# Performance work log

Hardware: AMD Instinct MI355X
Metric: run time of the kernel (lower is better)

Reference implementation:

```python
import jax, jax.numpy as jnp
import numpy as np

NUM_HEADS = 16
D_MODEL = 1024
D_K = D_MODEL // NUM_HEADS
EPS = 1e-6


def setup_inputs() -> dict:
    key = jax.random.key(0)
    ks = jax.random.split(key, 12)
    B, S, D = 8, 1024, D_MODEL
    scale = 0.02
    return {
        "query": jax.random.normal(ks[0], (B, S, D), dtype=jnp.float32),
        "key": jax.random.normal(ks[1], (B, S, D), dtype=jnp.float32),
        "value": jax.random.normal(ks[2], (B, S, D), dtype=jnp.float32),
        "policy": jax.random.uniform(ks[3], (B, S, 1), dtype=jnp.float32),
        "wq_w": jax.random.normal(ks[4], (D, D), dtype=jnp.float32) * scale,
        "wq_b": jnp.zeros((D,), dtype=jnp.float32),
        "wk_w": jax.random.normal(ks[5], (D, D), dtype=jnp.float32) * scale,
        "wk_b": jnp.zeros((D,), dtype=jnp.float32),
        "wv_w": jax.random.normal(ks[6], (D, D), dtype=jnp.float32) * scale,
        "wv_b": jnp.zeros((D,), dtype=jnp.float32),
        "dense_w": jax.random.normal(ks[7], (D, D), dtype=jnp.float32) * scale,
        "dense_b": jnp.zeros((D,), dtype=jnp.float32),
    }


def _split_heads(x):
    B, S, D = x.shape
    return x.reshape(B, S, NUM_HEADS, D_K).transpose(0, 2, 1, 3)  # [B,H,S,dk]


def reference(query, key, value, policy, wq_w, wq_b, wk_w, wk_b, wv_w, wv_b, dense_w, dense_b):
    B, S, D = query.shape
    # torch Linear: y = x @ W.T + b
    q = _split_heads(query @ wq_w.T + wq_b)
    k = _split_heads(key @ wk_w.T + wk_b)
    v = _split_heads(value @ wv_w.T + wv_b)

    scores = jnp.einsum("bhqd,bhkd->bhqk", q, k) / jnp.sqrt(jnp.float32(D_K))
    # policy branch: exp * policy normalization (no softmax max-subtraction, faithful)
    attn_policy = policy.reshape(B, 1, 1, S)
    sc = jnp.exp(scores) * attn_policy
    p_attn = (sc + EPS / S) / (jnp.sum(sc, axis=-1, keepdims=True) + EPS)

    x = jnp.einsum("bhqk,bhkd->bhqd", p_attn, v)
    x = x.transpose(0, 2, 1, 3).reshape(B, S, D)
    out = x @ dense_w.T + dense_b  # dropout = identity (eval mode)
    return out
```

## Files before the change

kernel.cpp:

```cpp
#include <hip/hip_runtime.h>


#define Sdim 1024
#define Ddim 1024

typedef unsigned short u16;
typedef float f32x4 __attribute__((ext_vector_type(4)));
typedef __bf16 bf16x8 __attribute__((ext_vector_type(8)));
typedef u16 u16x8 __attribute__((ext_vector_type(8)));
typedef __attribute__((address_space(3))) void lds_void;
typedef __attribute__((address_space(1))) void gbl_void;

__device__ __forceinline__ u16 f2bf(float f) {
    unsigned u = __float_as_uint(f);
    u += 0x7fffu + ((u >> 16) & 1u);
    return (u16)(u >> 16);
}
__device__ __forceinline__ void gld16(const void* g, void* l) {
    __builtin_amdgcn_global_load_lds((const gbl_void*)g, (lds_void*)l, 16, 0, 0);
}
#define MFMA16(a, b, c) __builtin_amdgcn_mfma_f32_16x16x32_bf16((a), (b), (c), 0, 0, 0)

__global__ __launch_bounds__(256) void cvt3(const float* __restrict__ s0,
                                            const float* __restrict__ s1,
                                            const float* __restrict__ s2,
                                            u16* __restrict__ d0,
                                            u16* __restrict__ d1,
                                            u16* __restrict__ d2) {
    const int z = blockIdx.y;
    const float* s = z == 0 ? s0 : z == 1 ? s1 : s2;
    u16* d = z == 0 ? d0 : z == 1 ? d1 : d2;
    const int i = (blockIdx.x * 256 + threadIdx.x) * 8;
    const float4 a = *(const float4*)(s + i);
    const float4 b = *(const float4*)(s + i + 4);
    u16x8 o;
    o[0] = f2bf(a.x); o[1] = f2bf(a.y); o[2] = f2bf(a.z); o[3] = f2bf(a.w);
    o[4] = f2bf(b.x); o[5] = f2bf(b.y); o[6] = f2bf(b.z); o[7] = f2bf(b.w);
    *(u16x8*)(d + i) = o;
}
__global__ __launch_bounds__(256) void cvt4(const float* __restrict__ s0,
                                            const float* __restrict__ s1,
                                            const float* __restrict__ s2,
                                            const float* __restrict__ s3,
                                            u16* __restrict__ d0,
                                            u16* __restrict__ d1,
                                            u16* __restrict__ d2,
                                            u16* __restrict__ d3) {
    const int z = blockIdx.y;
    const float* s = z == 0 ? s0 : z == 1 ? s1 : z == 2 ? s2 : s3;
    u16* d = z == 0 ? d0 : z == 1 ? d1 : z == 2 ? d2 : d3;
    const int i = (blockIdx.x * 256 + threadIdx.x) * 8;
    const float4 a = *(const float4*)(s + i);
    const float4 b = *(const float4*)(s + i + 4);
    u16x8 o;
    o[0] = f2bf(a.x); o[1] = f2bf(a.y); o[2] = f2bf(a.z); o[3] = f2bf(a.w);
    o[4] = f2bf(b.x); o[5] = f2bf(b.y); o[6] = f2bf(b.z); o[7] = f2bf(b.w);
    *(u16x8*)(d + i) = o;
}

template <bool OUT_BF16>
__device__ __forceinline__ void gemm_body(const u16* __restrict__ A,
                                          const u16* __restrict__ W,
                                          const float* __restrict__ bias,
                                          void* __restrict__ Cout,
                                          u16* As, u16* Bs,
                                          int m0, int n0) {
    const int tid  = threadIdx.x;
    const int wave = tid >> 6;
    const int lane = tid & 63;
    const int l15  = lane & 15;
    const int quad = lane >> 4;
    const int wm = (wave >> 1) * 64;
    const int wn = (wave & 1) * 64;

    const int e0 = wave * 512 + lane * 8;
    const int r0 = e0 >> 5, c0 = e0 & 31;
    const int e1 = 2048 + e0;
    const int r1 = e1 >> 5, c1 = e1 & 31;
    const u16* Ag0 = A + (size_t)(m0 + r0) * Ddim + c0;
    const u16* Ag1 = A + (size_t)(m0 + r1) * Ddim + c1;
    const u16* Wg0 = W + (size_t)(n0 + r0) * Ddim + c0;
    const u16* Wg1 = W + (size_t)(n0 + r1) * Ddim + c1;
    u16* As0 = As + wave * 512;
    u16* As1 = As + 2048 + wave * 512;
    u16* Bs0 = Bs + wave * 512;
    u16* Bs1 = Bs + 2048 + wave * 512;

    f32x4 acc[4][4] = {};

    for (int k0 = 0; k0 < Ddim; k0 += 32) {
        __syncthreads();
        gld16(Ag0 + k0, As0);
        gld16(Ag1 + k0, As1);
        gld16(Wg0 + k0, Bs0);
        gld16(Wg1 + k0, Bs1);
        __syncthreads();
        bf16x8 af[4], bfr[4];
#pragma unroll
        for (int i = 0; i < 4; ++i)
            af[i] = *(const bf16x8*)(As + (wm + i * 16 + l15) * 32 + quad * 8);
#pragma unroll
        for (int j = 0; j < 4; ++j)
            bfr[j] = *(const bf16x8*)(Bs + (wn + j * 16 + l15) * 32 + quad * 8);
#pragma unroll
        for (int i = 0; i < 4; ++i)
#pragma unroll
            for (int j = 0; j < 4; ++j)
                acc[i][j] = MFMA16(af[i], bfr[j], acc[i][j]);
    }

    float bv[4];
#pragma unroll
    for (int j = 0; j < 4; ++j) bv[j] = bias[n0 + wn + j * 16 + l15];
#pragma unroll
    for (int i = 0; i < 4; ++i)
#pragma unroll
        for (int j = 0; j < 4; ++j)
#pragma unroll
            for (int r = 0; r < 4; ++r) {
                const int row = m0 + wm + i * 16 + quad * 4 + r;
                const int col = n0 + wn + j * 16 + l15;
                const float v = acc[i][j][r] + bv[j];
                if (OUT_BF16)
                    ((u16*)Cout)[(size_t)row * Ddim + col] = f2bf(v);
                else
                    ((float*)Cout)[(size_t)row * Ddim + col] = v;
            }
}

__global__ __launch_bounds__(256) void gemm_qkv(const u16* __restrict__ A0, const u16* __restrict__ A1,
                                                const u16* __restrict__ A2,
                                                const u16* __restrict__ W0, const u16* __restrict__ W1,
                                                const u16* __restrict__ W2,
                                                const float* __restrict__ b0, const float* __restrict__ b1,
                                                const float* __restrict__ b2,
                                                u16* __restrict__ C0, u16* __restrict__ C1,
                                                u16* __restrict__ C2) {
    __shared__ __align__(16) u16 As[128 * 32];
    __shared__ __align__(16) u16 Bs[128 * 32];
    const int z = blockIdx.z;
    const u16* A = z == 0 ? A0 : z == 1 ? A1 : A2;
    const u16* W = z == 0 ? W0 : z == 1 ? W1 : W2;
    const float* bias = z == 0 ? b0 : z == 1 ? b1 : b2;
    u16* C = z == 0 ? C0 : z == 1 ? C1 : C2;
    gemm_body<true>(A, W, bias, (void*)C, As, Bs, blockIdx.x * 128, blockIdx.y * 128);
}

__global__ __launch_bounds__(256) void gemm_dense(const u16* __restrict__ A,
                                                  const u16* __restrict__ W,
                                                  const float* __restrict__ bias,
                                                  float* __restrict__ C) {
    __shared__ __align__(16) u16 As[128 * 32];
    __shared__ __align__(16) u16 Bs[128 * 32];
    gemm_body<false>(A, W, bias, (void*)C, As, Bs, blockIdx.x * 128, blockIdx.y * 128);
}

__global__ __launch_bounds__(256) void transp_v(const u16* __restrict__ Vp,
                                                u16* __restrict__ Vt) {
    __shared__ __align__(16) u16 Ts[64][72];
    const int bh = blockIdx.x, s0 = blockIdx.y * 64;
    const int b = bh >> 4, h = bh & 15;
    const int tid = threadIdx.x;
#pragma unroll
    for (int p = 0; p < 2; ++p) {
        const int e = p * 2048 + tid * 8;
        const int r = e >> 6, c = e & 63;
        *(u16x8*)&Ts[r][c] =
            *(const u16x8*)(Vp + ((size_t)(b * Sdim + s0 + r)) * Ddim + h * 64 + c);
    }
    __syncthreads();
    const int d = tid >> 2, sp = tid & 3;
#pragma unroll
    for (int g = 0; g < 2; ++g) {
        u16x8 o;
#pragma unroll
        for (int j = 0; j < 8; ++j) o[j] = Ts[sp * 16 + g * 8 + j][d];
        *(u16x8*)(Vt + ((size_t)(bh * 64 + d)) * Sdim + s0 + sp * 16 + g * 8) = o;
    }
}

__global__ __launch_bounds__(256) void attn_mfma(const u16* __restrict__ Qp,
                                                 const u16* __restrict__ Kp,
                                                 const u16* __restrict__ Vt,
                                                 const float* __restrict__ pol,
                                                 u16* __restrict__ Xb) {
    __shared__ __align__(16) u16 lds[29184];
    u16* Qs = lds;
    u16* Ks = lds + 4096;
    u16* Vs = lds + 12288;
    u16* Pg = lds + 20480;
    float* Xred = (float*)(lds + 4096);
    u16* XbR = lds + 20480;
    float* denb = (float*)(lds + 28672);
    float* pols = (float*)(lds + 28928);

    const int tid  = threadIdx.x;
    const int wave = tid >> 6;
    const int lane = tid & 63;
    const int l15  = lane & 15;
    const int quad = lane >> 4;
    const int wm = wave >> 1;
    const int wn = wave & 1;
    const int q0 = blockIdx.x * 64;
    const int bh = blockIdx.y;
    const int b = bh >> 4;
    const size_t bS = (size_t)b * Sdim;
    const int col0 = (bh & 15) * 64;
    const int lr4 = lane >> 2;
    const int lc8 = (lane & 3) * 8;

#pragma unroll
    for (int ks = 0; ks < 2; ++ks)
        gld16(Qp + (bS + q0 + wave * 16 + lr4) * Ddim + col0 + ks * 32 + lc8,
              Qs + (ks * 64 + wave * 16) * 32);

    f32x4 xacc[2][4] = {};
    float den[2][4] = {};

    for (int kt = 0; kt < 8; ++kt) {
        const int kbase = kt * 128;
        __syncthreads();
#pragma unroll
        for (int ks = 0; ks < 2; ++ks)
#pragma unroll
            for (int tt = 0; tt < 2; ++tt) {
                const int rblk = wave * 2 + tt;
                gld16(Kp + (bS + kbase + rblk * 16 + lr4) * Ddim + col0 + ks * 32 + lc8,
                      Ks + (ks * 128 + rblk * 16) * 32);
            }
#pragma unroll
        for (int tt = 0; tt < 4; ++tt)
            gld16(Vt + ((size_t)(bh * 64 + tt * 16 + lr4)) * Sdim + kbase + wave * 32 + lc8,
                  Vs + (wave * 64 + tt * 16) * 32);
        if (tid < 128) pols[tid] = pol[bS + kbase + tid];
        __syncthreads();

        bf16x8 aq[2][2];
#pragma unroll
        for (int i = 0; i < 2; ++i)
#pragma unroll
            for (int ks = 0; ks < 2; ++ks)
                aq[i][ks] = *(const bf16x8*)(Qs + (ks * 64 + wm * 32 + i * 16 + l15) * 32 + quad * 8);
#pragma unroll
        for (int i = 0; i < 2; ++i)
#pragma unroll
            for (int nt = 0; nt < 4; ++nt) {
                f32x4 sc = {};
#pragma unroll
                for (int ks = 0; ks < 2; ++ks) {
                    const bf16x8 bk =
                        *(const bf16x8*)(Ks + (ks * 128 + wn * 64 + nt * 16 + l15) * 32 + quad * 8);
                    sc = MFMA16(aq[i][ks], bk, sc);
                }
                const float pl = pols[wn * 64 + nt * 16 + l15];
#pragma unroll
                for (int r = 0; r < 4; ++r) {
                    const float p = __expf(sc[r] * 0.125f) * pl;
                    den[i][r] += p;
                    Pg[(((wave * 2 + i) * 2 + (nt >> 1)) * 16 + quad * 4 + r) * 32 +
                       (nt & 1) * 16 + l15] = f2bf(p);
                }
            }
#pragma unroll
        for (int i = 0; i < 2; ++i) {
            bf16x8 ap[2];
#pragma unroll
            for (int ks = 0; ks < 2; ++ks)
                ap[ks] = *(const bf16x8*)(Pg + (((wave * 2 + i) * 2 + ks) * 16 + l15) * 32 + quad * 8);
#pragma unroll
            for (int nd = 0; nd < 4; ++nd)
#pragma unroll
                for (int ks = 0; ks < 2; ++ks) {
                    const bf16x8 bv =
                        *(const bf16x8*)(Vs + ((wn * 2 + ks) * 64 + nd * 16 + l15) * 32 + quad * 8);
                    xacc[i][nd] = MFMA16(ap[ks], bv, xacc[i][nd]);
                }
        }
    }

    __syncthreads();

#pragma unroll
    for (int m = 1; m < 16; m <<= 1)
#pragma unroll
        for (int i = 0; i < 2; ++i)
#pragma unroll
            for (int r = 0; r < 4; ++r)
                den[i][r] += __shfl_xor(den[i][r], m, 64);
    if (l15 == 0)
#pragma unroll
        for (int i = 0; i < 2; ++i)
#pragma unroll
            for (int r = 0; r < 4; ++r)
                denb[wn * 64 + wm * 32 + i * 16 + quad * 4 + r] = den[i][r];
    if (wn == 1)
#pragma unroll
        for (int i = 0; i < 2; ++i)
#pragma unroll
            for (int nd = 0; nd < 4; ++nd)
#pragma unroll
                for (int r = 0; r < 4; ++r)
                    Xred[(wm * 32 + i * 16 + quad * 4 + r) * 68 + nd * 16 + l15] = xacc[i][nd][r];
    __syncthreads();

    if (wn == 0) {
#pragma unroll
        for (int i = 0; i < 2; ++i) {
            float inv[4];
#pragma unroll
            for (int r = 0; r < 4; ++r) {
                const int row = wm * 32 + i * 16 + quad * 4 + r;
                inv[r] = 1.0f / (denb[row] + denb[64 + row] + 1e-6f);
            }
#pragma unroll
            for (int nd = 0; nd < 4; ++nd)
#pragma unroll
                for (int r = 0; r < 4; ++r) {
                    const int row = wm * 32 + i * 16 + quad * 4 + r;
                    const float x = xacc[i][nd][r] + Xred[row * 68 + nd * 16 + l15];
                    XbR[row * 64 + nd * 16 + l15] = f2bf(x * inv[r]);
                }
        }
    }
    __syncthreads();

#pragma unroll
    for (int g = 0; g < 2; ++g) {
        const int e = g * 2048 + tid * 8;
        const int rr = e >> 6, cc = e & 63;
        const u16x8 o = *(const u16x8*)(XbR + rr * 64 + cc);
        *(u16x8*)(Xb + (bS + q0 + rr) * Ddim + col0 + cc) = o;
    }
}

extern "C" void kernel_launch(void* const* d_in, const int* in_sizes, int n_in,
                              void* d_out, int out_size, void* d_ws, size_t ws_size,
                              hipStream_t stream) {
    const float* query   = (const float*)d_in[0];
    const float* key     = (const float*)d_in[1];
    const float* value   = (const float*)d_in[2];
    const float* policy  = (const float*)d_in[3];
    const float* wq_w    = (const float*)d_in[4];
    const float* wq_b    = (const float*)d_in[5];
    const float* wk_w    = (const float*)d_in[6];
    const float* wk_b    = (const float*)d_in[7];
    const float* wv_w    = (const float*)d_in[8];
    const float* wv_b    = (const float*)d_in[9];
    const float* dense_w = (const float*)d_in[10];
    const float* dense_b = (const float*)d_in[11];

    const size_t MM = 1u << 20;
    const size_t A8 = 8 * MM;
    u16* qa  = (u16*)d_ws;
    u16* ka  = qa + A8;
    u16* va  = ka + A8;
    u16* wqb = va + A8;
    u16* wkb = wqb + MM;
    u16* wvb = wkb + MM;
    u16* wdb = wvb + MM;
    u16* Qp  = wdb + MM;
    u16* Kp  = Qp + A8;
    u16* Vp  = Kp + A8;
    u16* Vtg = ka;
    u16* Xb  = qa;

    cvt3<<<dim3(4096, 3), 256, 0, stream>>>(query, key, value, qa, ka, va);
    cvt4<<<dim3(512, 4), 256, 0, stream>>>(wq_w, wk_w, wv_w, dense_w, wqb, wkb, wvb, wdb);

    gemm_qkv<<<dim3(64, 8, 3), 256, 0, stream>>>(qa, ka, va, wqb, wkb, wvb,
                                                 wq_b, wk_b, wv_b, Qp, Kp, Vp);
    transp_v<<<dim3(128, 16), 256, 0, stream>>>(Vp, Vtg);

    attn_mfma<<<dim3(16, 128), 256, 0, stream>>>(Qp, Kp, Vtg, policy, Xb);

    gemm_dense<<<dim3(64, 8), 256, 0, stream>>>(Xb, wdb, dense_b, (float*)d_out);
}
```

Measured before the change: 353.8 us.

## Rework attention kernel with 32x32 MFMA, register-resident P and 256-row Q tiles

```diff
diff --git a/kernel.cpp b/kernel.cpp
--- a/kernel.cpp
+++ b/kernel.cpp
@@ -6,6 +6,7 @@
 
 typedef unsigned short u16;
 typedef float f32x4 __attribute__((ext_vector_type(4)));
+typedef float f32x16 __attribute__((ext_vector_type(16)));
 typedef __bf16 bf16x8 __attribute__((ext_vector_type(8)));
 typedef u16 u16x8 __attribute__((ext_vector_type(8)));
 typedef __attribute__((address_space(3))) void lds_void;
@@ -19,49 +20,45 @@
 __device__ __forceinline__ void gld16(const void* g, void* l) {
     __builtin_amdgcn_global_load_lds((const gbl_void*)g, (lds_void*)l, 16, 0, 0);
 }
+__device__ __forceinline__ unsigned pk_bf16(float lo, float hi) {
+    const unsigned ul = __float_as_uint(lo) + 0x8000u;
+    const unsigned uh = __float_as_uint(hi) + 0x8000u;
+    return __builtin_amdgcn_perm(uh, ul, 0x07060302u);
+}
 #define MFMA16(a, b, c) __builtin_amdgcn_mfma_f32_16x16x32_bf16((a), (b), (c), 0, 0, 0)
-
-__global__ __launch_bounds__(256) void cvt3(const float* __restrict__ s0,
-                                            const float* __restrict__ s1,
-                                            const float* __restrict__ s2,
-                                            u16* __restrict__ d0,
-                                            u16* __restrict__ d1,
-                                            u16* __restrict__ d2) {
+#define MFMA32(a, b, c) __builtin_amdgcn_mfma_f32_32x32x16_bf16((a), (b), (c), 0, 0, 0)
+
+__global__ __launch_bounds__(256) void cvt_all(const float* __restrict__ s0,
+                                               const float* __restrict__ s1,
+                                               const float* __restrict__ s2,
+                                               const float* __restrict__ s3,
+                                               const float* __restrict__ s4,
+                                               const float* __restrict__ s5,
+                                               const float* __restrict__ s6,
+                                               u16* __restrict__ d0, u16* __restrict__ d1,
+                                               u16* __restrict__ d2, u16* __restrict__ d3,
+                                               u16* __restrict__ d4, u16* __restrict__ d5,
+                                               u16* __restrict__ d6) {
     const int z = blockIdx.y;
-    const float* s = z == 0 ? s0 : z == 1 ? s1 : s2;
-    u16* d = z == 0 ? d0 : z == 1 ? d1 : d2;
+    if (z >= 3 && blockIdx.x >= 512) return;
+    const float* s = z == 0 ? s0 : z == 1 ? s1 : z == 2 ? s2 : z == 3 ? s3
+                   : z == 4 ? s4 : z == 5 ? s5 : s6;
+    u16* d = z == 0 ? d0 : z == 1 ? d1 : z == 2 ? d2 : z == 3 ? d3
+           : z == 4 ? d4 : z == 5 ? d5 : d6;
+    const float sc = (z == 3) ? 0.125f : 1.0f;
     const int i = (blockIdx.x * 256 + threadIdx.x) * 8;
     const float4 a = *(const float4*)(s + i);
     const float4 b = *(const float4*)(s + i + 4);
     u16x8 o;
-    o[0] = f2bf(a.x); o[1] = f2bf(a.y); o[2] = f2bf(a.z); o[3] = f2bf(a.w);
-    o[4] = f2bf(b.x); o[5] = f2bf(b.y); o[6] = f2bf(b.z); o[7] = f2bf(b.w);
-    *(u16x8*)(d + i) = o;
-}
-__global__ __launch_bounds__(256) void cvt4(const float* __restrict__ s0,
-                                            const float* __restrict__ s1,
-                                            const float* __restrict__ s2,
-                                            const float* __restrict__ s3,
-                                            u16* __restrict__ d0,
-                                            u16* __restrict__ d1,
-                                            u16* __restrict__ d2,
-                                            u16* __restrict__ d3) {
-    const int z = blockIdx.y;
-    const float* s = z == 0 ? s0 : z == 1 ? s1 : z == 2 ? s2 : s3;
-    u16* d = z == 0 ? d0 : z == 1 ? d1 : z == 2 ? d2 : d3;
-    const int i = (blockIdx.x * 256 + threadIdx.x) * 8;
-    const float4 a = *(const float4*)(s + i);
-    const float4 b = *(const float4*)(s + i + 4);
-    u16x8 o;
-    o[0] = f2bf(a.x); o[1] = f2bf(a.y); o[2] = f2bf(a.z); o[3] = f2bf(a.w);
-    o[4] = f2bf(b.x); o[5] = f2bf(b.y); o[6] = f2bf(b.z); o[7] = f2bf(b.w);
+    o[0] = f2bf(a.x * sc); o[1] = f2bf(a.y * sc); o[2] = f2bf(a.z * sc); o[3] = f2bf(a.w * sc);
+    o[4] = f2bf(b.x * sc); o[5] = f2bf(b.y * sc); o[6] = f2bf(b.z * sc); o[7] = f2bf(b.w * sc);
     *(u16x8*)(d + i) = o;
 }
 
 template <bool OUT_BF16>
 __device__ __forceinline__ void gemm_body(const u16* __restrict__ A,
                                           const u16* __restrict__ W,
-                                          const float* __restrict__ bias,
+                                          const float* __restrict__ bias, float bscale,
                                           void* __restrict__ Cout,
                                           u16* As, u16* Bs,
                                           int m0, int n0) {
@@ -111,7 +108,7 @@
 
     float bv[4];
 #pragma unroll
-    for (int j = 0; j < 4; ++j) bv[j] = bias[n0 + wn + j * 16 + l15];
+    for (int j = 0; j < 4; ++j) bv[j] = bias[n0 + wn + j * 16 + l15] * bscale;
 #pragma unroll
     for (int i = 0; i < 4; ++i)
 #pragma unroll
@@ -143,7 +140,8 @@
     const u16* W = z == 0 ? W0 : z == 1 ? W1 : W2;
     const float* bias = z == 0 ? b0 : z == 1 ? b1 : b2;
     u16* C = z == 0 ? C0 : z == 1 ? C1 : C2;
-    gemm_body<true>(A, W, bias, (void*)C, As, Bs, blockIdx.x * 128, blockIdx.y * 128);
+    const float bsc = (z == 0) ? 0.125f : 1.0f;
+    gemm_body<true>(A, W, bias, bsc, (void*)C, As, Bs, blockIdx.x * 128, blockIdx.y * 128);
 }
 
 __global__ __launch_bounds__(256) void gemm_dense(const u16* __restrict__ A,
@@ -152,7 +150,7 @@
                                                   float* __restrict__ C) {
     __shared__ __align__(16) u16 As[128 * 32];
     __shared__ __align__(16) u16 Bs[128 * 32];
-    gemm_body<false>(A, W, bias, (void*)C, As, Bs, blockIdx.x * 128, blockIdx.y * 128);
+    gemm_body<false>(A, W, bias, 1.0f, (void*)C, As, Bs, blockIdx.x * 128, blockIdx.y * 128);
 }
 
 __global__ __launch_bounds__(256) void transp_v(const u16* __restrict__ Vp,
@@ -179,157 +177,148 @@
     }
 }
 
-__global__ __launch_bounds__(256) void attn_mfma(const u16* __restrict__ Qp,
-                                                 const u16* __restrict__ Kp,
-                                                 const u16* __restrict__ Vt,
-                                                 const float* __restrict__ pol,
-                                                 u16* __restrict__ Xb) {
-    __shared__ __align__(16) u16 lds[29184];
+__global__ __launch_bounds__(256, 2) void attn_mfma(const u16* __restrict__ Qp,
+                                                    const u16* __restrict__ Kp,
+                                                    const u16* __restrict__ Vt,
+                                                    const float* __restrict__ pol,
+                                                    u16* __restrict__ Xb) {
+    __shared__ __align__(16) u16 lds[28288];
     u16* Qs = lds;
-    u16* Ks = lds + 4096;
-    u16* Vs = lds + 12288;
-    u16* Pg = lds + 20480;
-    float* Xred = (float*)(lds + 4096);
-    u16* XbR = lds + 20480;
-    float* denb = (float*)(lds + 28672);
-    float* pols = (float*)(lds + 28928);
+    u16* Ks = lds + 18432;
+    u16* Vs = lds + 23040;
+    float* pols = (float*)(lds + 27648);
+    float* denb = pols + 64;
 
     const int tid  = threadIdx.x;
-    const int wave = tid >> 6;
+    const int w    = tid >> 6;
     const int lane = tid & 63;
-    const int l15  = lane & 15;
-    const int quad = lane >> 4;
-    const int wm = wave >> 1;
-    const int wn = wave & 1;
-    const int q0 = blockIdx.x * 64;
+    const int l31  = lane & 31;
+    const unsigned hsel = lane >> 5;
+    const int q0 = blockIdx.x * 256;
     const int bh = blockIdx.y;
-    const int b = bh >> 4;
-    const size_t bS = (size_t)b * Sdim;
+    const size_t bS = (size_t)(bh >> 4) * Sdim;
     const int col0 = (bh & 15) * 64;
-    const int lr4 = lane >> 2;
-    const int lc8 = (lane & 3) * 8;
-
-#pragma unroll
-    for (int ks = 0; ks < 2; ++ks)
-        gld16(Qp + (bS + q0 + wave * 16 + lr4) * Ddim + col0 + ks * 32 + lc8,
-              Qs + (ks * 64 + wave * 16) * 32);
-
-    f32x4 xacc[2][4] = {};
-    float den[2][4] = {};
-
-    for (int kt = 0; kt < 8; ++kt) {
-        const int kbase = kt * 128;
+    const int sr = tid >> 2;
+    const int sc4 = tid & 3;
+
+#pragma unroll
+    for (int rg = 0; rg < 4; ++rg) {
+        const int r = rg * 64 + sr;
+#pragma unroll
+        for (int g = 0; g < 2; ++g) {
+            const int ch = sc4 + g * 4;
+            *(u16x8*)(Qs + r * 72 + ch * 8) =
+                *(const u16x8*)(Qp + (bS + q0 + r) * Ddim + col0 + ch * 8);
+        }
+    }
+    __syncthreads();
+    bf16x8 Qf[2][4];
+#pragma unroll
+    for (int qt = 0; qt < 2; ++qt)
+#pragma unroll
+        for (int dkt = 0; dkt < 4; ++dkt)
+            Qf[qt][dkt] = *(const bf16x8*)(Qs + (w * 64 + qt * 32 + l31) * 72 +
+                                           dkt * 16 + hsel * 8);
+
+    f32x16 X[2][2] = {};
+    float den[2] = {0.f, 0.f};
+
+    for (int kt = 0; kt < 16; ++kt) {
+        const int kbase = kt * 64;
         __syncthreads();
 #pragma unroll
-        for (int ks = 0; ks < 2; ++ks)
-#pragma unroll
-            for (int tt = 0; tt < 2; ++tt) {
-                const int rblk = wave * 2 + tt;
-                gld16(Kp + (bS + kbase + rblk * 16 + lr4) * Ddim + col0 + ks * 32 + lc8,
-                      Ks + (ks * 128 + rblk * 16) * 32);
-            }
-#pragma unroll
-        for (int tt = 0; tt < 4; ++tt)
-            gld16(Vt + ((size_t)(bh * 64 + tt * 16 + lr4)) * Sdim + kbase + wave * 32 + lc8,
-                  Vs + (wave * 64 + tt * 16) * 32);
-        if (tid < 128) pols[tid] = pol[bS + kbase + tid];
+        for (int g = 0; g < 2; ++g) {
+            const int ch = sc4 + g * 4;
+            *(u16x8*)(Ks + sr * 72 + ch * 8) =
+                *(const u16x8*)(Kp + (bS + kbase + sr) * Ddim + col0 + ch * 8);
+            *(u16x8*)(Vs + sr * 72 + ch * 8) =
+                *(const u16x8*)(Vt + ((size_t)(bh * 64 + sr)) * Sdim + kbase + ch * 8);
+        }
+        if (tid < 64) pols[tid] = pol[bS + kbase + tid];
         __syncthreads();
 
-        bf16x8 aq[2][2];
-#pragma unroll
-        for (int i = 0; i < 2; ++i)
-#pragma unroll
-            for (int ks = 0; ks < 2; ++ks)
-                aq[i][ks] = *(const bf16x8*)(Qs + (ks * 64 + wm * 32 + i * 16 + l15) * 32 + quad * 8);
-#pragma unroll
-        for (int i = 0; i < 2; ++i)
-#pragma unroll
-            for (int nt = 0; nt < 4; ++nt) {
-                f32x4 sc = {};
-#pragma unroll
-                for (int ks = 0; ks < 2; ++ks) {
-                    const bf16x8 bk =
-                        *(const bf16x8*)(Ks + (ks * 128 + wn * 64 + nt * 16 + l15) * 32 + quad * 8);
-                    sc = MFMA16(aq[i][ks], bk, sc);
+#pragma unroll
+        for (int t32 = 0; t32 < 2; ++t32) {
+            float polv[16];
+#pragma unroll
+            for (int e = 0; e < 16; ++e)
+                polv[e] = pols[t32 * 32 + (e & 3) + 8 * (e >> 2) + 4 * hsel];
+            bf16x8 Kf[4];
+#pragma unroll
+            for (int dkt = 0; dkt < 4; ++dkt)
+                Kf[dkt] = *(const bf16x8*)(Ks + (t32 * 32 + l31) * 72 +
+                                           dkt * 16 + hsel * 8);
+#pragma unroll
+            for (int qt = 0; qt < 2; ++qt) {
+                f32x16 S = {};
+#pragma unroll
+                for (int dkt = 0; dkt < 4; ++dkt)
+                    S = MFMA32(Kf[dkt], Qf[qt][dkt], S);
+                float p[16];
+#pragma unroll
+                for (int e = 0; e < 16; ++e) {
+                    p[e] = __expf(S[e]) * polv[e];
+                    den[qt] += p[e];
                 }
-                const float pl = pols[wn * 64 + nt * 16 + l15];
-#pragma unroll
-                for (int r = 0; r < 4; ++r) {
-                    const float p = __expf(sc[r] * 0.125f) * pl;
-                    den[i][r] += p;
-                    Pg[(((wave * 2 + i) * 2 + (nt >> 1)) * 16 + quad * 4 + r) * 32 +
-                       (nt & 1) * 16 + l15] = f2bf(p);
+                unsigned pk_[8], sw[8];
+#pragma unroll
+                for (int g = 0; g < 4; ++g) {
+                    pk_[2 * g]     = pk_bf16(p[4 * g + 0], p[4 * g + 1]);
+                    pk_[2 * g + 1] = pk_bf16(p[4 * g + 2], p[4 * g + 3]);
+                }
+#pragma unroll
+                for (int i = 0; i < 8; ++i)
+                    sw[i] = (unsigned)__shfl_xor((int)pk_[i], 32);
+#pragma unroll
+                for (int tau = 0; tau < 2; ++tau) {
+                    union { unsigned u[4]; bf16x8 v; } Af;
+                    Af.u[0] = hsel ? sw[(2 * tau + 1) * 2 + 0] : pk_[(2 * tau) * 2 + 0];
+                    Af.u[1] = hsel ? sw[(2 * tau + 1) * 2 + 1] : pk_[(2 * tau) * 2 + 1];
+                    Af.u[2] = hsel ? pk_[(2 * tau + 1) * 2 + 0] : sw[(2 * tau) * 2 + 0];
+                    Af.u[3] = hsel ? pk_[(2 * tau + 1) * 2 + 1] : sw[(2 * tau) * 2 + 1];
+#pragma unroll
+                    for (int ndt = 0; ndt < 2; ++ndt) {
+                        const bf16x8 Vf =
+                            *(const bf16x8*)(Vs + (ndt * 32 + l31) * 72 +
+                                             t32 * 32 + tau * 16 + hsel * 8);
+                        X[qt][ndt] = MFMA32(Af.v, Vf, X[qt][ndt]);
+                    }
                 }
             }
-#pragma unroll
-        for (int i = 0; i < 2; ++i) {
-            bf16x8 ap[2];
-#pragma unroll
-            for (int ks = 0; ks < 2; ++ks)
-                ap[ks] = *(const bf16x8*)(Pg + (((wave * 2 + i) * 2 + ks) * 16 + l15) * 32 + quad * 8);
-#pragma unroll
-            for (int nd = 0; nd < 4; ++nd)
-#pragma unroll
-                for (int ks = 0; ks < 2; ++ks) {
-                    const bf16x8 bv =
-                        *(const bf16x8*)(Vs + ((wn * 2 + ks) * 64 + nd * 16 + l15) * 32 + quad * 8);
-                    xacc[i][nd] = MFMA16(ap[ks], bv, xacc[i][nd]);
-                }
         }
     }
 
+#pragma unroll
+    for (int qt = 0; qt < 2; ++qt) {
+        den[qt] += __shfl_xor(den[qt], 32);
+        denb[w * 64 + qt * 32 + l31] = 1.0f / (den[qt] + 1e-6f);
+    }
+    u16* Xout = Qs;
+#pragma unroll
+    for (int qt = 0; qt < 2; ++qt) {
+        float invv[16];
+#pragma unroll
+        for (int e = 0; e < 16; ++e)
+            invv[e] = denb[w * 64 + qt * 32 + (e & 3) + 8 * (e >> 2) + 4 * hsel];
+#pragma unroll
+        for (int ndt = 0; ndt < 2; ++ndt)
+#pragma unroll
+            for (int e = 0; e < 16; ++e) {
+                const int rho = (e & 3) + 8 * (e >> 2) + 4 * hsel;
+                Xout[(w * 64 + qt * 32 + rho) * 72 + ndt * 32 + l31] =
+                    f2bf(X[qt][ndt][e] * invv[e]);
+            }
+    }
     __syncthreads();
-
-#pragma unroll
-    for (int m = 1; m < 16; m <<= 1)
-#pragma unroll
-        for (int i = 0; i < 2; ++i)
-#pragma unroll
-            for (int r = 0; r < 4; ++r)
-                den[i][r] += __shfl_xor(den[i][r], m, 64);
-    if (l15 == 0)
-#pragma unroll
-        for (int i = 0; i < 2; ++i)
-#pragma unroll
-            for (int r = 0; r < 4; ++r)
-                denb[wn * 64 + wm * 32 + i * 16 + quad * 4 + r] = den[i][r];
-    if (wn == 1)
-#pragma unroll
-        for (int i = 0; i < 2; ++i)
-#pragma unroll
-            for (int nd = 0; nd < 4; ++nd)
-#pragma unroll
-                for (int r = 0; r < 4; ++r)
-                    Xred[(wm * 32 + i * 16 + quad * 4 + r) * 68 + nd * 16 + l15] = xacc[i][nd][r];
-    __syncthreads();
-
-    if (wn == 0) {
-#pragma unroll
-        for (int i = 0; i < 2; ++i) {
-            float inv[4];
-#pragma unroll
-            for (int r = 0; r < 4; ++r) {
-                const int row = wm * 32 + i * 16 + quad * 4 + r;
-                inv[r] = 1.0f / (denb[row] + denb[64 + row] + 1e-6f);
-            }
-#pragma unroll
-            for (int nd = 0; nd < 4; ++nd)
-#pragma unroll
-                for (int r = 0; r < 4; ++r) {
-                    const int row = wm * 32 + i * 16 + quad * 4 + r;
-                    const float x = xacc[i][nd][r] + Xred[row * 68 + nd * 16 + l15];
-                    XbR[row * 64 + nd * 16 + l15] = f2bf(x * inv[r]);
-                }
+#pragma unroll
+    for (int rg = 0; rg < 4; ++rg) {
+        const int r = rg * 64 + sr;
+#pragma unroll
+        for (int g = 0; g < 2; ++g) {
+            const int ch = sc4 + g * 4;
+            *(u16x8*)(Xb + (bS + q0 + r) * Ddim + col0 + ch * 8) =
+                *(const u16x8*)(Xout + r * 72 + ch * 8);
         }
-    }
-    __syncthreads();
-
-#pragma unroll
-    for (int g = 0; g < 2; ++g) {
-        const int e = g * 2048 + tid * 8;
-        const int rr = e >> 6, cc = e & 63;
-        const u16x8 o = *(const u16x8*)(XbR + rr * 64 + cc);
-        *(u16x8*)(Xb + (bS + q0 + rr) * Ddim + col0 + cc) = o;
     }
 }
 
@@ -364,14 +353,14 @@
     u16* Vtg = ka;
     u16* Xb  = qa;
 
-    cvt3<<<dim3(4096, 3), 256, 0, stream>>>(query, key, value, qa, ka, va);
-    cvt4<<<dim3(512, 4), 256, 0, stream>>>(wq_w, wk_w, wv_w, dense_w, wqb, wkb, wvb, wdb);
+    cvt_all<<<dim3(4096, 7), 256, 0, stream>>>(query, key, value, wq_w, wk_w, wv_w, dense_w,
+                                               qa, ka, va, wqb, wkb, wvb, wdb);
 
     gemm_qkv<<<dim3(64, 8, 3), 256, 0, stream>>>(qa, ka, va, wqb, wkb, wvb,
                                                  wq_b, wk_b, wv_b, Qp, Kp, Vp);
     transp_v<<<dim3(128, 16), 256, 0, stream>>>(Vp, Vtg);
 
-    attn_mfma<<<dim3(16, 128), 256, 0, stream>>>(Qp, Kp, Vtg, policy, Xb);
+    attn_mfma<<<dim3(4, 128), 256, 0, stream>>>(Qp, Kp, Vtg, policy, Xb);
 
     gemm_dense<<<dim3(64, 8), 256, 0, stream>>>(Xb, wdb, dense_b, (float*)d_out);
 }
```

After: 309.2 us. 1.14x faster.
